# Optimization experiments

Measured on AMD Instinct MI355X. Metric: run time of the kernel, lower is better.

Reference implementation:

```python
import jax, jax.numpy as jnp
import numpy as np
import math

B, T, IN, H, OUT, L = 8, 256, 128, 128, 128, 2
MAX_EP_LEN = 10000.0


def _rotate(x, pos, d):
    # rope as in source: repeat(1,1,2) = concat along last dim (not interleave)
    half = jnp.exp(jnp.arange(0, d, 2, dtype=jnp.float32) * (-math.log(MAX_EP_LEN) / d))  # [d/2]
    ang = pos[..., None] * half  # [B,T,d/2]
    sine = jnp.concatenate([jnp.sin(ang), jnp.sin(ang)], axis=-1)
    cos = jnp.concatenate([jnp.cos(ang), jnp.cos(ang)], axis=-1)
    y1, y2 = jnp.split(x, 2, axis=-1)
    x_rot = jnp.concatenate([-y2, y1], axis=-1)
    return x * cos + x_rot * sine


def _layernorm(x, w, b, eps=1e-5):
    m = jnp.mean(x, axis=-1, keepdims=True)
    v = jnp.mean((x - m) ** 2, axis=-1, keepdims=True)
    return (x - m) / jnp.sqrt(v + eps) * w + b


def _block(x, S0, Z0, Wk, Wq, Wv, lw, lb, w1, b1, w2, b2, scw, scb):
    # x: [B,T,F]; S0: [B,F,F]; Z0: [B,F]
    x = _layernorm(x, lw, lb)
    K = jax.nn.elu(x @ Wk.T) + 1.0
    Q = jax.nn.elu(x @ Wq.T) + 1.0
    V = x @ Wv.T
    outer = jnp.einsum('bti,btj->btij', K, V)  # [B,T,F,F]
    S = jnp.clip(jnp.cumsum(outer, axis=1), -1e20, 1e20) + S0[:, None]  # [B,T,F,F]
    Z = jnp.clip(jnp.cumsum(K, axis=1), -1e20, 1e20) + Z0[:, None]      # [B,T,F]
    num = jnp.einsum('bti,btil->btl', Q, S)
    den = jnp.einsum('bti,bti->bt', Q, Z)[..., None] + 1e-5
    out = num / den
    out = jax.nn.relu(jax.nn.relu(out @ w1.T + b1) @ w2.T + b2)  # feed_forward
    out = out + x @ scw.T + scb                                   # residual shortcut
    return out, S[:, -1], Z[:, -1]


def setup_inputs() -> dict:
    key = jax.random.key(0)
    ks = jax.random.split(key, 14)
    s = 0.05
    return {
        'z': jax.random.normal(ks[0], (T, B, IN), jnp.float32),
        'state': jnp.zeros((B, L * (H * H + H) + 1), jnp.float32),
        'Wk': jax.random.normal(ks[1], (L, H, IN), jnp.float32) * s,
        'Wq': jax.random.normal(ks[2], (L, H, IN), jnp.float32) * s,
        'Wv': jax.random.normal(ks[3], (L, H, IN), jnp.float32) * s,
        'ln_w': jnp.ones((L, IN), jnp.float32),
        'ln_b': jnp.zeros((L, IN), jnp.float32),
        'ff_w1': jax.random.normal(ks[4], (L, H, H), jnp.float32) * s,
        'ff_b1': jnp.zeros((L, H), jnp.float32),
        'ff_w2': jax.random.normal(ks[5], (L, H, H), jnp.float32) * s,
        'ff_b2': jnp.zeros((L, H), jnp.float32),
        'sc_w': jax.random.normal(ks[6], (L, H, IN), jnp.float32) * s,
        'sc_b': jnp.zeros((L, H), jnp.float32),
        'unmap_w': jax.random.normal(ks[7], (OUT, H), jnp.float32) * s,
        'unmap_b': jnp.zeros((OUT,), jnp.float32),
    }


def reference(z, state, Wk, Wq, Wv, ln_w, ln_b, ff_w1, ff_b1, ff_w2, ff_b2, sc_w, sc_b, unmap_w, unmap_b):
    x = jnp.transpose(z, (1, 0, 2))  # [B,T,IN]
    ts = state[:, -1]                # [B] timestep counters
    core = state[:, :-1].reshape(B, L, H * H + H)
    pos = ts[:, None] + jnp.arange(T, dtype=jnp.float32)[None, :]  # [B,T]
    x = _rotate(x, pos, IN)  # embedding_type == 'rope'
    new_states = []
    for i in range(L):
        S0 = core[:, i, :H * H].reshape(B, H, H)
        Z0 = core[:, i, H * H:]
        x, Sl, Zl = _block(x, S0, Z0, Wk[i], Wq[i], Wv[i], ln_w[i], ln_b[i],
                           ff_w1[i], ff_b1[i], ff_w2[i], ff_b2[i], sc_w[i], sc_b[i])
        new_states.append(jnp.concatenate([Sl.reshape(B, -1), Zl], axis=-1))
    y = x @ unmap_w.T + unmap_b
    st = jnp.concatenate([jnp.stack(new_states, axis=1).reshape(B, -1), (ts + T)[:, None]], axis=-1)
    return jnp.transpose(y, (1, 0, 2)), st
```

## Files before the change

kernel.cpp:

```cpp
#include <hip/hip_runtime.h>
#include <math.h>

#define Bn 8
#define Tn 256
#define COREn 16512
#define SDn   33025

typedef __attribute__((ext_vector_type(8))) short short8;
typedef __attribute__((ext_vector_type(4))) short short4v;
typedef __attribute__((ext_vector_type(4))) float floatx4;

#define MFMA16(a,b,c) __builtin_amdgcn_mfma_f32_16x16x32_bf16(a,b,c,0,0,0)

static __device__ __forceinline__ unsigned short f2bf(float f) {
  unsigned int u = __float_as_uint(f);
  return (unsigned short)((u + 0x7FFFu + ((u >> 16) & 1u)) >> 16);
}
static __device__ __forceinline__ float bf2f(unsigned short h) {
  return __uint_as_float((unsigned int)h << 16);
}
static __device__ __forceinline__ short8 ldwfrag(const float* p) {
  float4 a = *(const float4*)p;
  float4 b = *(const float4*)(p + 4);
  short8 r;
  r[0] = (short)f2bf(a.x); r[1] = (short)f2bf(a.y);
  r[2] = (short)f2bf(a.z); r[3] = (short)f2bf(a.w);
  r[4] = (short)f2bf(b.x); r[5] = (short)f2bf(b.y);
  r[6] = (short)f2bf(b.z); r[7] = (short)f2bf(b.w);
  return r;
}
static __device__ __forceinline__ void ld8(const float* p, float* v) {
  float4 a = *(const float4*)p, b = *(const float4*)(p + 4);
  v[0]=a.x; v[1]=a.y; v[2]=a.z; v[3]=a.w; v[4]=b.x; v[5]=b.y; v[6]=b.z; v[7]=b.w;
}

struct Phase1 {
  unsigned short Ssc[4][16][40];
  float Obuf[4][16][132];
  float denw[4][16];
};
struct Phase2 {
  float sk[16][132];
  float os[16][132];
};
struct Smem {
  unsigned short xs[16][136];
  unsigned short xattn[16][136];
  unsigned short hs[16][136];
  float Z0s[128];
  float denz[16];
  float dinv[16];
  union { Phase1 p1; Phase2 p2; } u;
};

static __device__ __forceinline__ void proj_epilogue(
    int by, int g0, int b, int t0l, int n0, int n1, int quad,
    floatx4 acc0, floatx4 acc1,
    unsigned short* __restrict__ Kb, unsigned short* __restrict__ Kt,
    unsigned short* __restrict__ Qb, unsigned short* __restrict__ Vt,
    float* __restrict__ skipb, const float* __restrict__ scb) {
  if (by == 0) {
    short4v kt0, kt1;
#pragma unroll
    for (int j = 0; j < 4; j++) {
      int row = quad * 4 + j;
      float e0 = acc0[j] > 0.f ? acc0[j] + 1.f : expf(acc0[j]);
      float e1 = acc1[j] > 0.f ? acc1[j] + 1.f : expf(acc1[j]);
      Kb[(size_t)(g0 + row) * 128 + n0] = f2bf(e0);
      Kb[(size_t)(g0 + row) * 128 + n1] = f2bf(e1);
      kt0[j] = (short)f2bf(e0); kt1[j] = (short)f2bf(e1);
    }
    *(short4v*)(Kt + (size_t)(b * 128 + n0) * 256 + t0l + quad * 4) = kt0;
    *(short4v*)(Kt + (size_t)(b * 128 + n1) * 256 + t0l + quad * 4) = kt1;
  } else if (by == 1) {
#pragma unroll
    for (int j = 0; j < 4; j++) {
      int row = quad * 4 + j;
      float e0 = acc0[j] > 0.f ? acc0[j] + 1.f : expf(acc0[j]);
      float e1 = acc1[j] > 0.f ? acc1[j] + 1.f : expf(acc1[j]);
      Qb[(size_t)(g0 + row) * 128 + n0] = f2bf(e0);
      Qb[(size_t)(g0 + row) * 128 + n1] = f2bf(e1);
    }
  } else if (by == 2) {
    short4v v0, v1;
#pragma unroll
    for (int j = 0; j < 4; j++) { v0[j] = (short)f2bf(acc0[j]); v1[j] = (short)f2bf(acc1[j]); }
    *(short4v*)(Vt + (size_t)(b * 128 + n0) * 256 + t0l + quad * 4) = v0;
    *(short4v*)(Vt + (size_t)(b * 128 + n1) * 256 + t0l + quad * 4) = v1;
  } else {
    float sb0 = scb[n0], sb1 = scb[n1];
#pragma unroll
    for (int j = 0; j < 4; j++) {
      int row = quad * 4 + j;
      skipb[(size_t)(g0 + row) * 128 + n0] = acc0[j] + sb0;
      skipb[(size_t)(g0 + row) * 128 + n1] = acc1[j] + sb1;
    }
  }
}

static __device__ void attn_ff(
    Smem& s, int tid, int b, int rt, int l,
    const unsigned short* __restrict__ Kb, const unsigned short* __restrict__ Qb,
    const unsigned short* __restrict__ Vt,
    const float* __restrict__ state, const float* __restrict__ skipin,
    const float* __restrict__ w1, const float* __restrict__ b1,
    const float* __restrict__ w2, const float* __restrict__ b2,
    const float* __restrict__ Wk1, const float* __restrict__ Wq1,
    const float* __restrict__ Wv1, const float* __restrict__ scw1,
    const float* __restrict__ lnw1, const float* __restrict__ lnb1,
    const float* __restrict__ scb1,
    unsigned short* __restrict__ Kb1, unsigned short* __restrict__ Kt1,
    unsigned short* __restrict__ Qb1, unsigned short* __restrict__ Vt1,
    float* __restrict__ skip1,
    const float* __restrict__ unw, const float* __restrict__ unb,
    float* __restrict__ yout) {
  const int lane = tid & 63, wv = tid >> 6, lm = lane & 15, quad = lane >> 4;
  const int t0 = rt * 16;
  const size_t sb = (size_t)b * SDn + (size_t)l * COREn;

  { int r = tid >> 4, c = (tid & 15) * 8;
    *(short8*)&s.xs[r][c] = *(const short8*)(Qb + (size_t)(b * 256 + t0 + r) * 128 + c); }
  if (tid < 128) s.Z0s[tid] = state[sb + 16384 + tid];
  __syncthreads();

  { int r = tid >> 4, c = (tid & 15) * 8;
    float qz = 0.f;
#pragma unroll
    for (int i = 0; i < 8; i++) qz += bf2f(s.xs[r][c + i]) * s.Z0s[c + i];
    for (int d = 8; d; d >>= 1) qz += __shfl_xor(qz, d, 16);
    if ((tid & 15) == 0) s.denz[r] = qz; }

  floatx4 oacc[8];
#pragma unroll
  for (int jt = 0; jt < 8; jt++) oacc[jt] = floatx4{0.f, 0.f, 0.f, 0.f};
  float dacc[4] = {0.f, 0.f, 0.f, 0.f};

  const int nch = rt / 2 + 1;
  for (int c = wv; c < nch; c += 4) {
    const int kb = c * 32;
    floatx4 s0 = {0.f,0.f,0.f,0.f}, s1 = {0.f,0.f,0.f,0.f};
#pragma unroll
    for (int kc = 0; kc < 4; kc++) {
      short8 a  = *(const short8*)&s.xs[lm][kc * 32 + quad * 8];
      short8 k0 = *(const short8*)(Kb + (size_t)(b * 256 + kb + lm) * 128 + kc * 32 + quad * 8);
      short8 k1 = *(const short8*)(Kb + (size_t)(b * 256 + kb + 16 + lm) * 128 + kc * 32 + quad * 8);
      s0 = MFMA16(a, k0, s0);
      s1 = MFMA16(a, k1, s1);
    }
    const int tau0 = kb + lm, tau1 = kb + 16 + lm;
#pragma unroll
    for (int j = 0; j < 4; j++) {
      int m = t0 + quad * 4 + j;
      float v0 = (tau0 <= m) ? s0[j] : 0.f;
      float v1 = (tau1 <= m) ? s1[j] : 0.f;
      dacc[j] += v0 + v1;
      s.u.p1.Ssc[wv][quad * 4 + j][lm]      = f2bf(v0);
      s.u.p1.Ssc[wv][quad * 4 + j][16 + lm] = f2bf(v1);
    }
    short8 sa = *(const short8*)&s.u.p1.Ssc[wv][lm][quad * 8];
#pragma unroll
    for (int jt = 0; jt < 8; jt++) {
      short8 vb = *(const short8*)(Vt + (size_t)(b * 128 + jt * 16 + lm) * 256 + kb + quad * 8);
      oacc[jt] = MFMA16(sa, vb, oacc[jt]);
    }
  }

  { const float* S0 = state + sb;
    short8 aq = *(const short8*)&s.xs[lm][wv * 32 + quad * 8];
#pragma unroll
    for (int jt = 0; jt < 8; jt++) {
      short8 vb;
#pragma unroll
      for (int jj = 0; jj < 8; jj++)
        vb[jj] = (short)f2bf(S0[(size_t)(wv * 32 + quad * 8 + jj) * 128 + jt * 16 + lm]);
      oacc[jt] = MFMA16(aq, vb, oacc[jt]);
    } }

#pragma unroll
  for (int j = 0; j < 4; j++)
    for (int d = 8; d; d >>= 1) dacc[j] += __shfl_xor(dacc[j], d, 16);
  if (lm == 0) {
#pragma unroll
    for (int j = 0; j < 4; j++) s.u.p1.denw[wv][quad * 4 + j] = dacc[j];
  }
#pragma unroll
  for (int jt = 0; jt < 8; jt++)
#pragma unroll
    for (int j = 0; j < 4; j++)
      s.u.p1.Obuf[wv][quad * 4 + j][jt * 16 + lm] = oacc[jt][j];
  __syncthreads();
  if (tid < 16)
    s.dinv[tid] = 1.f / (s.denz[tid] + s.u.p1.denw[0][tid] + s.u.p1.denw[1][tid]
                         + s.u.p1.denw[2][tid] + s.u.p1.denw[3][tid] + 1e-5f);
  __syncthreads();
  { int r = tid >> 4, c = (tid & 15) * 8;
    float di = s.dinv[r];
    short8 ov;
#pragma unroll
    for (int i = 0; i < 8; i++) {
      float o = s.u.p1.Obuf[0][r][c + i] + s.u.p1.Obuf[1][r][c + i]
              + s.u.p1.Obuf[2][r][c + i] + s.u.p1.Obuf[3][r][c + i];
      ov[i] = (short)f2bf(o * di);
    }
    *(short8*)&s.xattn[r][c] = ov; }
  __syncthreads();

  const int gr0 = b * 256 + t0;
#pragma unroll
  for (int p = 0; p < 2; p++) {
    int f = tid + p * 256;
    int rr = f >> 5, cc = (f & 31) * 4;
    *(float4*)&s.u.p2.sk[rr][cc] = *(const float4*)(skipin + (size_t)(gr0 + rr) * 128 + cc);
  }
  const int n0 = wv * 32 + lm, n1 = n0 + 16;

  { floatx4 a0 = {0.f,0.f,0.f,0.f}, a1 = {0.f,0.f,0.f,0.f};
#pragma unroll
    for (int kc = 0; kc < 4; kc++) {
      short8 a  = *(const short8*)&s.xattn[lm][kc * 32 + quad * 8];
      short8 bA = ldwfrag(w1 + (size_t)n0 * 128 + kc * 32 + quad * 8);
      short8 bB = ldwfrag(w1 + (size_t)n1 * 128 + kc * 32 + quad * 8);
      a0 = MFMA16(a, bA, a0);
      a1 = MFMA16(a, bB, a1);
    }
    float bi0 = b1[n0], bi1 = b1[n1];
#pragma unroll
    for (int j = 0; j < 4; j++) {
      int row = quad * 4 + j;
      s.hs[row][n0] = f2bf(fmaxf(a0[j] + bi0, 0.f));
      s.hs[row][n1] = f2bf(fmaxf(a1[j] + bi1, 0.f));
    } }
  __syncthreads();

  float o0[4], o1[4];
  { floatx4 a0 = {0.f,0.f,0.f,0.f}, a1 = {0.f,0.f,0.f,0.f};
#pragma unroll
    for (int kc = 0; kc < 4; kc++) {
      short8 a  = *(const short8*)&s.hs[lm][kc * 32 + quad * 8];
      short8 bA = ldwfrag(w2 + (size_t)n0 * 128 + kc * 32 + quad * 8);
      short8 bB = ldwfrag(w2 + (size_t)n1 * 128 + kc * 32 + quad * 8);
      a0 = MFMA16(a, bA, a0);
      a1 = MFMA16(a, bB, a1);
    }
    float bi0 = b2[n0], bi1 = b2[n1];
#pragma unroll
    for (int j = 0; j < 4; j++) {
      int row = quad * 4 + j;
      o0[j] = fmaxf(a0[j] + bi0, 0.f) + s.u.p2.sk[row][n0];
      o1[j] = fmaxf(a1[j] + bi1, 0.f) + s.u.p2.sk[row][n1];
    } }

  if (l == 0) {
#pragma unroll
    for (int j = 0; j < 4; j++) {
      int row = quad * 4 + j;
      s.u.p2.os[row][n0] = o0[j];
      s.u.p2.os[row][n1] = o1[j];
    }
    __syncthreads();
    { int r = tid >> 4, c0 = (tid & 15) * 8;
      float v[8];
#pragma unroll
      for (int i = 0; i < 8; i++) v[i] = s.u.p2.os[r][c0 + i];
      float sm = 0.f, sq = 0.f;
#pragma unroll
      for (int i = 0; i < 8; i++) { sm += v[i]; sq += v[i] * v[i]; }
      for (int d = 8; d; d >>= 1) { sm += __shfl_xor(sm, d, 16); sq += __shfl_xor(sq, d, 16); }
      float mean = sm * (1.f / 128.f);
      float rstd = rsqrtf(sq * (1.f / 128.f) - mean * mean + 1e-5f);
      short8 xv;
#pragma unroll
      for (int i = 0; i < 8; i++)
        xv[i] = (short)f2bf((v[i] - mean) * rstd * lnw1[c0 + i] + lnb1[c0 + i]);
      *(short8*)&s.xs[r][c0] = xv; }
    __syncthreads();
#pragma unroll
    for (int by = 0; by < 4; by++) {
      const float* W = by == 0 ? Wk1 : by == 1 ? Wq1 : by == 2 ? Wv1 : scw1;
      floatx4 a0 = {0.f,0.f,0.f,0.f}, a1 = {0.f,0.f,0.f,0.f};
#pragma unroll
      for (int kc = 0; kc < 4; kc++) {
        short8 a  = *(const short8*)&s.xs[lm][kc * 32 + quad * 8];
        short8 bA = ldwfrag(W + (size_t)n0 * 128 + kc * 32 + quad * 8);
        short8 bB = ldwfrag(W + (size_t)n1 * 128 + kc * 32 + quad * 8);
        a0 = MFMA16(a, bA, a0);
        a1 = MFMA16(a, bB, a1);
      }
      proj_epilogue(by, gr0, b, t0, n0, n1, quad, a0, a1,
                    Kb1, Kt1, Qb1, Vt1, skip1, scb1);
    }
  } else {
#pragma unroll
    for (int j = 0; j < 4; j++) {
      int row = quad * 4 + j;
      s.xs[row][n0] = f2bf(o0[j]);
      s.xs[row][n1] = f2bf(o1[j]);
    }
    __syncthreads();
    floatx4 a0 = {0.f,0.f,0.f,0.f}, a1 = {0.f,0.f,0.f,0.f};
#pragma unroll
    for (int kc = 0; kc < 4; kc++) {
      short8 a  = *(const short8*)&s.xs[lm][kc * 32 + quad * 8];
      short8 bA = ldwfrag(unw + (size_t)n0 * 128 + kc * 32 + quad * 8);
      short8 bB = ldwfrag(unw + (size_t)n1 * 128 + kc * 32 + quad * 8);
      a0 = MFMA16(a, bA, a0);
      a1 = MFMA16(a, bB, a1);
    }
    float u0 = unb[n0], u1 = unb[n1];
#pragma unroll
    for (int j = 0; j < 4; j++) {
      int gg = gr0 + quad * 4 + j;
      int bb = gg >> 8, tq = gg & 255;
      yout[(size_t)(tq * Bn + bb) * 128 + n0] = a0[j] + u0;
      yout[(size_t)(tq * Bn + bb) * 128 + n1] = a1[j] + u1;
    }
  }
}

static __device__ void state_upd(
    int tid, int idx, int l,
    const unsigned short* __restrict__ Kt, const unsigned short* __restrict__ Vt,
    const float* __restrict__ state, float* __restrict__ st_out) {
  const int lane = tid & 63, wv = tid >> 6, lm = lane & 15, quad = lane >> 4;
  const int b = idx >> 4, sub = idx & 15;
  const int i0 = (sub >> 1) * 16, j0 = (sub & 1) * 64;
  const size_t sb = (size_t)b * SDn + (size_t)l * COREn;
  floatx4 acc = {0.f, 0.f, 0.f, 0.f};
#pragma unroll
  for (int kc = 0; kc < 8; kc++) {
    short8 ka = *(const short8*)(Kt + (size_t)(b * 128 + i0 + lm) * 256 + kc * 32 + quad * 8);
    short8 vb = *(const short8*)(Vt + (size_t)(b * 128 + j0 + wv * 16 + lm) * 256 + kc * 32 + quad * 8);
    acc = MFMA16(ka, vb, acc);
  }
#pragma unroll
  for (int j = 0; j < 4; j++) {
    size_t off = sb + (size_t)(i0 + quad * 4 + j) * 128 + j0 + wv * 16 + lm;
    st_out[off] = acc[j] + state[off];
  }
  if (j0 == 0) {
    if (tid < 128) {
      int i = tid >> 3, seg = tid & 7;
      const unsigned short* kr = Kt + (size_t)(b * 128 + i0 + i) * 256 + seg * 32;
      float zs = 0.f;
#pragma unroll
      for (int x = 0; x < 4; x++) {
        short8 kv = *(const short8*)(kr + x * 8);
#pragma unroll
        for (int y = 0; y < 8; y++) zs += bf2f((unsigned short)kv[y]);
      }
      for (int d = 4; d; d >>= 1) zs += __shfl_xor(zs, d, 8);
      if (seg == 0) {
        size_t zo = sb + 16384 + i0 + i;
        st_out[zo] = zs + state[zo];
      }
    }
    if (sub == 0 && tid == 0 && l == 0)
      st_out[(size_t)b * SDn + SDn - 1] = state[(size_t)b * SDn + SDn - 1] + 256.f;
  }
}

__global__ __launch_bounds__(256) void proj0_kernel(
    const float* __restrict__ z, const float* __restrict__ state,
    const float* __restrict__ Wk, const float* __restrict__ Wq,
    const float* __restrict__ Wv, const float* __restrict__ scw,
    const float* __restrict__ lnw, const float* __restrict__ lnb,
    const float* __restrict__ scb,
    unsigned short* __restrict__ Kb0, unsigned short* __restrict__ Qb0,
    unsigned short* __restrict__ Kt0, unsigned short* __restrict__ Vt0,
    float* __restrict__ skip0) {
  __shared__ unsigned short xs[16][136];
  const int tid = threadIdx.x, bx = blockIdx.x;
  const int lane = tid & 63, wv = tid >> 6, lm = lane & 15, quad = lane >> 4;
  const int tile = bx >> 1, half = bx & 1;
  const int g0 = tile * 16;
  const int r = tid >> 4, c0 = (tid & 15) * 8;
  const int g = g0 + r, b = g >> 8, t = g & 255;
  float v[8], pv[8];
  const float* zr = z + ((size_t)t * Bn + b) * 128;
  ld8(zr + c0, v);
  ld8(zr + (c0 ^ 64), pv);
  float pos = state[(size_t)b * SDn + SDn - 1] + (float)t;
#pragma unroll
  for (int i = 0; i < 8; i++) {
    int jj = (c0 + i) & 63;
    float ang = pos * expf((float)jj * -0.14391156831212787f);
    float sn = sinf(ang), cs = cosf(ang);
    v[i] = (c0 < 64) ? (v[i] * cs - pv[i] * sn) : (v[i] * cs + pv[i] * sn);
  }
  float sm = 0.f, sq = 0.f;
#pragma unroll
  for (int i = 0; i < 8; i++) { sm += v[i]; sq += v[i] * v[i]; }
  for (int d = 8; d; d >>= 1) { sm += __shfl_xor(sm, d, 16); sq += __shfl_xor(sq, d, 16); }
  float mean = sm * (1.f / 128.f);
  float rstd = rsqrtf(sq * (1.f / 128.f) - mean * mean + 1e-5f);
  short8 xv;
#pragma unroll
  for (int i = 0; i < 8; i++)
    xv[i] = (short)f2bf((v[i] - mean) * rstd * lnw[c0 + i] + lnb[c0 + i]);
  *(short8*)&xs[r][c0] = xv;
  __syncthreads();

  const int bb = g0 >> 8, t0l = g0 & 255;
  const int n0 = wv * 32 + lm, n1 = n0 + 16;
#pragma unroll
  for (int which = 0; which < 2; which++) {
    const float* W = half == 0 ? (which == 0 ? Wk : Wq)
                               : (which == 0 ? Wv : scw);
    floatx4 a0 = {0.f,0.f,0.f,0.f}, a1 = {0.f,0.f,0.f,0.f};
#pragma unroll
    for (int kc = 0; kc < 4; kc++) {
      short8 a  = *(const short8*)&xs[lm][kc * 32 + quad * 8];
      short8 bA = ldwfrag(W + (size_t)n0 * 128 + kc * 32 + quad * 8);
      short8 bB = ldwfrag(W + (size_t)n1 * 128 + kc * 32 + quad * 8);
      a0 = MFMA16(a, bA, a0);
      a1 = MFMA16(a, bB, a1);
    }
    proj_epilogue(half * 2 + which, g0, bb, t0l, n0, n1, quad, a0, a1,
                  Kb0, Kt0, Qb0, Vt0, skip0, scb);
  }
}

__global__ __launch_bounds__(256) void layer0_kernel(
    const unsigned short* __restrict__ Kb0, const unsigned short* __restrict__ Qb0,
    const unsigned short* __restrict__ Kt0, const unsigned short* __restrict__ Vt0,
    const float* __restrict__ skip0, const float* __restrict__ state,
    const float* __restrict__ w1, const float* __restrict__ b1,
    const float* __restrict__ w2, const float* __restrict__ b2,
    const float* __restrict__ Wk1, const float* __restrict__ Wq1,
    const float* __restrict__ Wv1, const float* __restrict__ scw1,
    const float* __restrict__ lnw1, const float* __restrict__ lnb1,
    const float* __restrict__ scb1,
    unsigned short* __restrict__ Kb1, unsigned short* __restrict__ Kt1,
    unsigned short* __restrict__ Qb1, unsigned short* __restrict__ Vt1,
    float* __restrict__ skip1, float* __restrict__ st_out) {
  __shared__ Smem s;
  const int tid = threadIdx.x, bx = blockIdx.x;
  if (bx < 128)
    attn_ff(s, tid, bx >> 4, bx & 15, 0,
            Kb0, Qb0, Vt0, state, skip0,
            w1, b1, w2, b2,
            Wk1, Wq1, Wv1, scw1, lnw1, lnb1, scb1,
            Kb1, Kt1, Qb1, Vt1, skip1,
            nullptr, nullptr, nullptr);
  else
    state_upd(tid, bx - 128, 0, Kt0, Vt0, state, st_out);
}

__global__ __launch_bounds__(256) void layer1_kernel(
    const unsigned short* __restrict__ Kb1, const unsigned short* __restrict__ Qb1,
    const unsigned short* __restrict__ Kt1, const unsigned short* __restrict__ Vt1,
    const float* __restrict__ skip1, const float* __restrict__ state,
    const float* __restrict__ w1, const float* __restrict__ b1,
    const float* __restrict__ w2, const float* __restrict__ b2,
    const float* __restrict__ unw, const float* __restrict__ unb,
    float* __restrict__ yout, float* __restrict__ st_out) {
  __shared__ Smem s;
  const int tid = threadIdx.x, bx = blockIdx.x;
  if (bx < 128)
    attn_ff(s, tid, bx >> 4, bx & 15, 1,
            Kb1, Qb1, Vt1, state, skip1,
            w1, b1, w2, b2,
            nullptr, nullptr, nullptr, nullptr, nullptr, nullptr, nullptr,
            nullptr, nullptr, nullptr, nullptr, nullptr,
            unw, unb, yout);
  else
    state_upd(tid, bx - 128, 1, Kt1, Vt1, state, st_out);
}

extern "C" void kernel_launch(void* const* d_in, const int* in_sizes, int n_in,
                              void* d_out, int out_size, void* d_ws, size_t ws_size,
                              hipStream_t stream) {
  const float* z       = (const float*)d_in[0];
  const float* state   = (const float*)d_in[1];
  const float* Wk      = (const float*)d_in[2];
  const float* Wq      = (const float*)d_in[3];
  const float* Wv      = (const float*)d_in[4];
  const float* ln_w    = (const float*)d_in[5];
  const float* ln_b    = (const float*)d_in[6];
  const float* ff_w1   = (const float*)d_in[7];
  const float* ff_b1   = (const float*)d_in[8];
  const float* ff_w2   = (const float*)d_in[9];
  const float* ff_b2   = (const float*)d_in[10];
  const float* sc_w    = (const float*)d_in[11];
  const float* sc_b    = (const float*)d_in[12];
  const float* unmap_w = (const float*)d_in[13];
  const float* unmap_b = (const float*)d_in[14];

  float* y_out  = (float*)d_out;
  float* st_out = y_out + (size_t)Tn * Bn * 128;

  const size_t E = 262144;
  unsigned short* Kb0 = (unsigned short*)d_ws;
  unsigned short* Qb0 = Kb0 + E;
  unsigned short* Kt0 = Qb0 + E;
  unsigned short* Vt0 = Kt0 + E;
  unsigned short* Kb1 = Vt0 + E;
  unsigned short* Qb1 = Kb1 + E;
  unsigned short* Kt1 = Qb1 + E;
  unsigned short* Vt1 = Kt1 + E;
  float* skip0 = (float*)(Vt1 + E);
  float* skip1 = skip0 + E;

  proj0_kernel<<<256, 256, 0, stream>>>(
      z, state, Wk, Wq, Wv, sc_w, ln_w, ln_b, sc_b,
      Kb0, Qb0, Kt0, Vt0, skip0);

  layer0_kernel<<<256, 256, 0, stream>>>(
      Kb0, Qb0, Kt0, Vt0, skip0, state,
      ff_w1, ff_b1, ff_w2, ff_b2,
      Wk + 16384, Wq + 16384, Wv + 16384, sc_w + 16384,
      ln_w + 128, ln_b + 128, sc_b + 128,
      Kb1, Kt1, Qb1, Vt1, skip1, st_out);

  layer1_kernel<<<256, 256, 0, stream>>>(
      Kb1, Qb1, Kt1, Vt1, skip1, state,
      ff_w1 + 16384, ff_b1 + 128, ff_w2 + 16384, ff_b2 + 128,
      unmap_w, unmap_b, y_out, st_out);
}
```

Baseline: 135.6 us.

## Split layer kernels into finer stages with more blocks and bf16 intermediates

Restructures the pipeline from three fat kernels into six stages: prep (rope+LN+projection plus a transposed bf16 copy of S0), attention split across two output-column halves, a separate feed-forward+LN kernel, a separate layer-1 projection kernel, and a fused FF+unmap kernel. The aim is more blocks per launch for better GPU occupancy, coalesced pre-transposed S0 reads instead of strided fp32 gathers, and bf16 skip storage to cut memory traffic. In exchange it adds more kernel launches, duplicates the QK score computation across the two halves, and round-trips attention output through global memory.

Result: faster. 130.4 us (-3.8%).

```diff
diff --git a/kernel.cpp b/kernel.cpp
--- a/kernel.cpp
+++ b/kernel.cpp
@@ -34,31 +34,12 @@
   v[0]=a.x; v[1]=a.y; v[2]=a.z; v[3]=a.w; v[4]=b.x; v[5]=b.y; v[6]=b.z; v[7]=b.w;
 }
 
-struct Phase1 {
-  unsigned short Ssc[4][16][40];
-  float Obuf[4][16][132];
-  float denw[4][16];
-};
-struct Phase2 {
-  float sk[16][132];
-  float os[16][132];
-};
-struct Smem {
-  unsigned short xs[16][136];
-  unsigned short xattn[16][136];
-  unsigned short hs[16][136];
-  float Z0s[128];
-  float denz[16];
-  float dinv[16];
-  union { Phase1 p1; Phase2 p2; } u;
-};
-
 static __device__ __forceinline__ void proj_epilogue(
     int by, int g0, int b, int t0l, int n0, int n1, int quad,
     floatx4 acc0, floatx4 acc1,
     unsigned short* __restrict__ Kb, unsigned short* __restrict__ Kt,
     unsigned short* __restrict__ Qb, unsigned short* __restrict__ Vt,
-    float* __restrict__ skipb, const float* __restrict__ scb) {
+    unsigned short* __restrict__ skipb, const float* __restrict__ scb) {
   if (by == 0) {
     short4v kt0, kt1;
 #pragma unroll
@@ -92,228 +73,88 @@
 #pragma unroll
     for (int j = 0; j < 4; j++) {
       int row = quad * 4 + j;
-      skipb[(size_t)(g0 + row) * 128 + n0] = acc0[j] + sb0;
-      skipb[(size_t)(g0 + row) * 128 + n1] = acc1[j] + sb1;
-    }
-  }
-}
-
-static __device__ void attn_ff(
-    Smem& s, int tid, int b, int rt, int l,
-    const unsigned short* __restrict__ Kb, const unsigned short* __restrict__ Qb,
-    const unsigned short* __restrict__ Vt,
-    const float* __restrict__ state, const float* __restrict__ skipin,
-    const float* __restrict__ w1, const float* __restrict__ b1,
-    const float* __restrict__ w2, const float* __restrict__ b2,
-    const float* __restrict__ Wk1, const float* __restrict__ Wq1,
-    const float* __restrict__ Wv1, const float* __restrict__ scw1,
-    const float* __restrict__ lnw1, const float* __restrict__ lnb1,
-    const float* __restrict__ scb1,
-    unsigned short* __restrict__ Kb1, unsigned short* __restrict__ Kt1,
-    unsigned short* __restrict__ Qb1, unsigned short* __restrict__ Vt1,
-    float* __restrict__ skip1,
-    const float* __restrict__ unw, const float* __restrict__ unb,
-    float* __restrict__ yout) {
-  const int lane = tid & 63, wv = tid >> 6, lm = lane & 15, quad = lane >> 4;
-  const int t0 = rt * 16;
-  const size_t sb = (size_t)b * SDn + (size_t)l * COREn;
-
-  { int r = tid >> 4, c = (tid & 15) * 8;
-    *(short8*)&s.xs[r][c] = *(const short8*)(Qb + (size_t)(b * 256 + t0 + r) * 128 + c); }
-  if (tid < 128) s.Z0s[tid] = state[sb + 16384 + tid];
-  __syncthreads();
-
-  { int r = tid >> 4, c = (tid & 15) * 8;
-    float qz = 0.f;
-#pragma unroll
-    for (int i = 0; i < 8; i++) qz += bf2f(s.xs[r][c + i]) * s.Z0s[c + i];
-    for (int d = 8; d; d >>= 1) qz += __shfl_xor(qz, d, 16);
-    if ((tid & 15) == 0) s.denz[r] = qz; }
-
-  floatx4 oacc[8];
-#pragma unroll
-  for (int jt = 0; jt < 8; jt++) oacc[jt] = floatx4{0.f, 0.f, 0.f, 0.f};
-  float dacc[4] = {0.f, 0.f, 0.f, 0.f};
-
-  const int nch = rt / 2 + 1;
-  for (int c = wv; c < nch; c += 4) {
-    const int kb = c * 32;
-    floatx4 s0 = {0.f,0.f,0.f,0.f}, s1 = {0.f,0.f,0.f,0.f};
+      skipb[(size_t)(g0 + row) * 128 + n0] = f2bf(acc0[j] + sb0);
+      skipb[(size_t)(g0 + row) * 128 + n1] = f2bf(acc1[j] + sb1);
+    }
+  }
+}
+
+__global__ __launch_bounds__(256) void prep_kernel(
+    const float* __restrict__ z, const float* __restrict__ state,
+    const float* __restrict__ Wk, const float* __restrict__ Wq,
+    const float* __restrict__ Wv, const float* __restrict__ scw,
+    const float* __restrict__ lnw, const float* __restrict__ lnb,
+    const float* __restrict__ scb,
+    unsigned short* __restrict__ Kb0, unsigned short* __restrict__ Qb0,
+    unsigned short* __restrict__ Kt0, unsigned short* __restrict__ Vt0,
+    unsigned short* __restrict__ skip0, unsigned short* __restrict__ S0t) {
+  const int tid = threadIdx.x, bx = blockIdx.x;
+  if (bx < 512) {
+    __shared__ unsigned short xs[16][136];
+    const int lane = tid & 63, wv = tid >> 6, lm = lane & 15, quad = lane >> 4;
+    const int tile = bx >> 2, by = bx & 3;
+    const int g0 = tile * 16;
+    const int r = tid >> 4, c0 = (tid & 15) * 8;
+    const int g = g0 + r, b = g >> 8, t = g & 255;
+    float v[8], pv[8];
+    const float* zr = z + ((size_t)t * Bn + b) * 128;
+    ld8(zr + c0, v);
+    ld8(zr + (c0 ^ 64), pv);
+    float pos = state[(size_t)b * SDn + SDn - 1] + (float)t;
+#pragma unroll
+    for (int i = 0; i < 8; i++) {
+      int jj = (c0 + i) & 63;
+      float ang = pos * expf((float)jj * -0.14391156831212787f);
+      float sn = sinf(ang), cs = cosf(ang);
+      v[i] = (c0 < 64) ? (v[i] * cs - pv[i] * sn) : (v[i] * cs + pv[i] * sn);
+    }
+    float sm = 0.f, sq = 0.f;
+#pragma unroll
+    for (int i = 0; i < 8; i++) { sm += v[i]; sq += v[i] * v[i]; }
+    for (int d = 8; d; d >>= 1) { sm += __shfl_xor(sm, d, 16); sq += __shfl_xor(sq, d, 16); }
+    float mean = sm * (1.f / 128.f);
+    float rstd = rsqrtf(sq * (1.f / 128.f) - mean * mean + 1e-5f);
+    short8 xv;
+#pragma unroll
+    for (int i = 0; i < 8; i++)
+      xv[i] = (short)f2bf((v[i] - mean) * rstd * lnw[c0 + i] + lnb[c0 + i]);
+    *(short8*)&xs[r][c0] = xv;
+    __syncthreads();
+
+    const float* W = by == 0 ? Wk : by == 1 ? Wq : by == 2 ? Wv : scw;
+    const int bb = g0 >> 8, t0l = g0 & 255;
+    const int n0 = wv * 32 + lm, n1 = n0 + 16;
+    floatx4 a0 = {0.f,0.f,0.f,0.f}, a1 = {0.f,0.f,0.f,0.f};
 #pragma unroll
     for (int kc = 0; kc < 4; kc++) {
-      short8 a  = *(const short8*)&s.xs[lm][kc * 32 + quad * 8];
-      short8 k0 = *(const short8*)(Kb + (size_t)(b * 256 + kb + lm) * 128 + kc * 32 + quad * 8);
-      short8 k1 = *(const short8*)(Kb + (size_t)(b * 256 + kb + 16 + lm) * 128 + kc * 32 + quad * 8);
-      s0 = MFMA16(a, k0, s0);
-      s1 = MFMA16(a, k1, s1);
-    }
-    const int tau0 = kb + lm, tau1 = kb + 16 + lm;
-#pragma unroll
-    for (int j = 0; j < 4; j++) {
-      int m = t0 + quad * 4 + j;
-      float v0 = (tau0 <= m) ? s0[j] : 0.f;
-      float v1 = (tau1 <= m) ? s1[j] : 0.f;
-      dacc[j] += v0 + v1;
-      s.u.p1.Ssc[wv][quad * 4 + j][lm]      = f2bf(v0);
-      s.u.p1.Ssc[wv][quad * 4 + j][16 + lm] = f2bf(v1);
-    }
-    short8 sa = *(const short8*)&s.u.p1.Ssc[wv][lm][quad * 8];
-#pragma unroll
-    for (int jt = 0; jt < 8; jt++) {
-      short8 vb = *(const short8*)(Vt + (size_t)(b * 128 + jt * 16 + lm) * 256 + kb + quad * 8);
-      oacc[jt] = MFMA16(sa, vb, oacc[jt]);
-    }
-  }
-
-  { const float* S0 = state + sb;
-    short8 aq = *(const short8*)&s.xs[lm][wv * 32 + quad * 8];
-#pragma unroll
-    for (int jt = 0; jt < 8; jt++) {
-      short8 vb;
-#pragma unroll
-      for (int jj = 0; jj < 8; jj++)
-        vb[jj] = (short)f2bf(S0[(size_t)(wv * 32 + quad * 8 + jj) * 128 + jt * 16 + lm]);
-      oacc[jt] = MFMA16(aq, vb, oacc[jt]);
-    } }
-
-#pragma unroll
-  for (int j = 0; j < 4; j++)
-    for (int d = 8; d; d >>= 1) dacc[j] += __shfl_xor(dacc[j], d, 16);
-  if (lm == 0) {
-#pragma unroll
-    for (int j = 0; j < 4; j++) s.u.p1.denw[wv][quad * 4 + j] = dacc[j];
-  }
-#pragma unroll
-  for (int jt = 0; jt < 8; jt++)
-#pragma unroll
-    for (int j = 0; j < 4; j++)
-      s.u.p1.Obuf[wv][quad * 4 + j][jt * 16 + lm] = oacc[jt][j];
-  __syncthreads();
-  if (tid < 16)
-    s.dinv[tid] = 1.f / (s.denz[tid] + s.u.p1.denw[0][tid] + s.u.p1.denw[1][tid]
-                         + s.u.p1.denw[2][tid] + s.u.p1.denw[3][tid] + 1e-5f);
-  __syncthreads();
-  { int r = tid >> 4, c = (tid & 15) * 8;
-    float di = s.dinv[r];
-    short8 ov;
-#pragma unroll
-    for (int i = 0; i < 8; i++) {
-      float o = s.u.p1.Obuf[0][r][c + i] + s.u.p1.Obuf[1][r][c + i]
-              + s.u.p1.Obuf[2][r][c + i] + s.u.p1.Obuf[3][r][c + i];
-      ov[i] = (short)f2bf(o * di);
-    }
-    *(short8*)&s.xattn[r][c] = ov; }
-  __syncthreads();
-
-  const int gr0 = b * 256 + t0;
-#pragma unroll
-  for (int p = 0; p < 2; p++) {
-    int f = tid + p * 256;
-    int rr = f >> 5, cc = (f & 31) * 4;
-    *(float4*)&s.u.p2.sk[rr][cc] = *(const float4*)(skipin + (size_t)(gr0 + rr) * 128 + cc);
-  }
-  const int n0 = wv * 32 + lm, n1 = n0 + 16;
-
-  { floatx4 a0 = {0.f,0.f,0.f,0.f}, a1 = {0.f,0.f,0.f,0.f};
-#pragma unroll
-    for (int kc = 0; kc < 4; kc++) {
-      short8 a  = *(const short8*)&s.xattn[lm][kc * 32 + quad * 8];
-      short8 bA = ldwfrag(w1 + (size_t)n0 * 128 + kc * 32 + quad * 8);
-      short8 bB = ldwfrag(w1 + (size_t)n1 * 128 + kc * 32 + quad * 8);
+      short8 a  = *(const short8*)&xs[lm][kc * 32 + quad * 8];
+      short8 bA = ldwfrag(W + (size_t)n0 * 128 + kc * 32 + quad * 8);
+      short8 bB = ldwfrag(W + (size_t)n1 * 128 + kc * 32 + quad * 8);
       a0 = MFMA16(a, bA, a0);
       a1 = MFMA16(a, bB, a1);
     }
-    float bi0 = b1[n0], bi1 = b1[n1];
-#pragma unroll
-    for (int j = 0; j < 4; j++) {
-      int row = quad * 4 + j;
-      s.hs[row][n0] = f2bf(fmaxf(a0[j] + bi0, 0.f));
-      s.hs[row][n1] = f2bf(fmaxf(a1[j] + bi1, 0.f));
-    } }
-  __syncthreads();
-
-  float o0[4], o1[4];
-  { floatx4 a0 = {0.f,0.f,0.f,0.f}, a1 = {0.f,0.f,0.f,0.f};
-#pragma unroll
-    for (int kc = 0; kc < 4; kc++) {
-      short8 a  = *(const short8*)&s.hs[lm][kc * 32 + quad * 8];
-      short8 bA = ldwfrag(w2 + (size_t)n0 * 128 + kc * 32 + quad * 8);
-      short8 bB = ldwfrag(w2 + (size_t)n1 * 128 + kc * 32 + quad * 8);
-      a0 = MFMA16(a, bA, a0);
-      a1 = MFMA16(a, bB, a1);
-    }
-    float bi0 = b2[n0], bi1 = b2[n1];
-#pragma unroll
-    for (int j = 0; j < 4; j++) {
-      int row = quad * 4 + j;
-      o0[j] = fmaxf(a0[j] + bi0, 0.f) + s.u.p2.sk[row][n0];
-      o1[j] = fmaxf(a1[j] + bi1, 0.f) + s.u.p2.sk[row][n1];
-    } }
-
-  if (l == 0) {
-#pragma unroll
-    for (int j = 0; j < 4; j++) {
-      int row = quad * 4 + j;
-      s.u.p2.os[row][n0] = o0[j];
-      s.u.p2.os[row][n1] = o1[j];
-    }
-    __syncthreads();
-    { int r = tid >> 4, c0 = (tid & 15) * 8;
-      float v[8];
-#pragma unroll
-      for (int i = 0; i < 8; i++) v[i] = s.u.p2.os[r][c0 + i];
-      float sm = 0.f, sq = 0.f;
-#pragma unroll
-      for (int i = 0; i < 8; i++) { sm += v[i]; sq += v[i] * v[i]; }
-      for (int d = 8; d; d >>= 1) { sm += __shfl_xor(sm, d, 16); sq += __shfl_xor(sq, d, 16); }
-      float mean = sm * (1.f / 128.f);
-      float rstd = rsqrtf(sq * (1.f / 128.f) - mean * mean + 1e-5f);
-      short8 xv;
-#pragma unroll
-      for (int i = 0; i < 8; i++)
-        xv[i] = (short)f2bf((v[i] - mean) * rstd * lnw1[c0 + i] + lnb1[c0 + i]);
-      *(short8*)&s.xs[r][c0] = xv; }
-    __syncthreads();
-#pragma unroll
-    for (int by = 0; by < 4; by++) {
-      const float* W = by == 0 ? Wk1 : by == 1 ? Wq1 : by == 2 ? Wv1 : scw1;
-      floatx4 a0 = {0.f,0.f,0.f,0.f}, a1 = {0.f,0.f,0.f,0.f};
-#pragma unroll
-      for (int kc = 0; kc < 4; kc++) {
-        short8 a  = *(const short8*)&s.xs[lm][kc * 32 + quad * 8];
-        short8 bA = ldwfrag(W + (size_t)n0 * 128 + kc * 32 + quad * 8);
-        short8 bB = ldwfrag(W + (size_t)n1 * 128 + kc * 32 + quad * 8);
-        a0 = MFMA16(a, bA, a0);
-        a1 = MFMA16(a, bB, a1);
+    proj_epilogue(by, g0, bb, t0l, n0, n1, quad, a0, a1,
+                  Kb0, Kt0, Qb0, Vt0, skip0, scb);
+  } else {
+    __shared__ float tl[32][33];
+    const int id = bx - 512, b = id >> 1, l = id & 1;
+    const float* src = state + (size_t)b * SDn + (size_t)l * COREn;
+    unsigned short* dst = S0t + (size_t)(l * 8 + b) * 16384;
+    const int r = tid >> 3, c4 = (tid & 7) * 4;
+#pragma unroll
+    for (int tI = 0; tI < 4; tI++)
+      for (int tJ = 0; tJ < 4; tJ++) {
+        int i0 = tI * 32, j0 = tJ * 32;
+#pragma unroll
+        for (int q = 0; q < 4; q++)
+          tl[r][c4 + q] = src[(size_t)(i0 + r) * 128 + j0 + c4 + q];
+        __syncthreads();
+        short4v o;
+#pragma unroll
+        for (int q = 0; q < 4; q++) o[q] = (short)f2bf(tl[c4 + q][r]);
+        *(short4v*)(dst + (size_t)(j0 + r) * 128 + i0 + c4) = o;
+        __syncthreads();
       }
-      proj_epilogue(by, gr0, b, t0, n0, n1, quad, a0, a1,
-                    Kb1, Kt1, Qb1, Vt1, skip1, scb1);
-    }
-  } else {
-#pragma unroll
-    for (int j = 0; j < 4; j++) {
-      int row = quad * 4 + j;
-      s.xs[row][n0] = f2bf(o0[j]);
-      s.xs[row][n1] = f2bf(o1[j]);
-    }
-    __syncthreads();
-    floatx4 a0 = {0.f,0.f,0.f,0.f}, a1 = {0.f,0.f,0.f,0.f};
-#pragma unroll
-    for (int kc = 0; kc < 4; kc++) {
-      short8 a  = *(const short8*)&s.xs[lm][kc * 32 + quad * 8];
-      short8 bA = ldwfrag(unw + (size_t)n0 * 128 + kc * 32 + quad * 8);
-      short8 bB = ldwfrag(unw + (size_t)n1 * 128 + kc * 32 + quad * 8);
-      a0 = MFMA16(a, bA, a0);
-      a1 = MFMA16(a, bB, a1);
-    }
-    float u0 = unb[n0], u1 = unb[n1];
-#pragma unroll
-    for (int j = 0; j < 4; j++) {
-      int gg = gr0 + quad * 4 + j;
-      int bb = gg >> 8, tq = gg & 255;
-      yout[(size_t)(tq * Bn + bb) * 128 + n0] = a0[j] + u0;
-      yout[(size_t)(tq * Bn + bb) * 128 + n1] = a1[j] + u1;
-    }
   }
 }
 
@@ -359,112 +200,310 @@
   }
 }
 
-__global__ __launch_bounds__(256) void proj0_kernel(
-    const float* __restrict__ z, const float* __restrict__ state,
+__global__ __launch_bounds__(256) void attn_kernel(
+    const unsigned short* __restrict__ Kb, const unsigned short* __restrict__ Qb,
+    const unsigned short* __restrict__ Vt, const unsigned short* __restrict__ Kt,
+    const unsigned short* __restrict__ S0tl, const float* __restrict__ state,
+    unsigned short* __restrict__ attnb, float* __restrict__ st_out, int l) {
+  const int tid = threadIdx.x, bx = blockIdx.x;
+  const int lane = tid & 63, wv = tid >> 6, lm = lane & 15, quad = lane >> 4;
+  if (bx < 256) {
+    __shared__ unsigned short xs[16][136];
+    __shared__ unsigned short Ssc[4][16][40];
+    __shared__ float Obuf[4][16][68];
+    __shared__ float Z0s[128];
+    __shared__ float denw[4][16];
+    __shared__ float denz[16];
+    __shared__ float dinv[16];
+
+    const int tile = bx >> 1, half = bx & 1;
+    const int b = tile >> 4, rt = tile & 15, t0 = rt * 16;
+    const size_t sb = (size_t)b * SDn + (size_t)l * COREn;
+    { int r = tid >> 4, c = (tid & 15) * 8;
+      *(short8*)&xs[r][c] = *(const short8*)(Qb + (size_t)(b * 256 + t0 + r) * 128 + c); }
+    if (tid < 128) Z0s[tid] = state[sb + 16384 + tid];
+    __syncthreads();
+
+    { int r = tid >> 4, c = (tid & 15) * 8;
+      float qz = 0.f;
+#pragma unroll
+      for (int i = 0; i < 8; i++) qz += bf2f(xs[r][c + i]) * Z0s[c + i];
+      for (int d = 8; d; d >>= 1) qz += __shfl_xor(qz, d, 16);
+      if ((tid & 15) == 0) denz[r] = qz; }
+
+    floatx4 oacc[4];
+#pragma unroll
+    for (int jt = 0; jt < 4; jt++) oacc[jt] = floatx4{0.f, 0.f, 0.f, 0.f};
+    float dacc[4] = {0.f, 0.f, 0.f, 0.f};
+
+    const int nch = rt / 2 + 1;
+    for (int c = wv; c < nch; c += 4) {
+      const int kb = c * 32;
+      short8 vfr[4];
+#pragma unroll
+      for (int jt = 0; jt < 4; jt++)
+        vfr[jt] = *(const short8*)(Vt + (size_t)(b * 128 + half * 64 + jt * 16 + lm) * 256 + kb + quad * 8);
+      floatx4 s0 = {0.f,0.f,0.f,0.f}, s1 = {0.f,0.f,0.f,0.f};
+#pragma unroll
+      for (int kc = 0; kc < 4; kc++) {
+        short8 a  = *(const short8*)&xs[lm][kc * 32 + quad * 8];
+        short8 k0 = *(const short8*)(Kb + (size_t)(b * 256 + kb + lm) * 128 + kc * 32 + quad * 8);
+        short8 k1 = *(const short8*)(Kb + (size_t)(b * 256 + kb + 16 + lm) * 128 + kc * 32 + quad * 8);
+        s0 = MFMA16(a, k0, s0);
+        s1 = MFMA16(a, k1, s1);
+      }
+      const int tau0 = kb + lm, tau1 = kb + 16 + lm;
+#pragma unroll
+      for (int j = 0; j < 4; j++) {
+        int m = t0 + quad * 4 + j;
+        float v0 = (tau0 <= m) ? s0[j] : 0.f;
+        float v1 = (tau1 <= m) ? s1[j] : 0.f;
+        dacc[j] += v0 + v1;
+        Ssc[wv][quad * 4 + j][lm]      = f2bf(v0);
+        Ssc[wv][quad * 4 + j][16 + lm] = f2bf(v1);
+      }
+      short8 sa = *(const short8*)&Ssc[wv][lm][quad * 8];
+#pragma unroll
+      for (int jt = 0; jt < 4; jt++)
+        oacc[jt] = MFMA16(sa, vfr[jt], oacc[jt]);
+    }
+
+    { short8 aq = *(const short8*)&xs[lm][wv * 32 + quad * 8];
+#pragma unroll
+      for (int jt = 0; jt < 4; jt++) {
+        short8 vb = *(const short8*)(S0tl + (size_t)b * 16384 +
+                        (size_t)(half * 64 + jt * 16 + lm) * 128 + wv * 32 + quad * 8);
+        oacc[jt] = MFMA16(aq, vb, oacc[jt]);
+      } }
+
+#pragma unroll
+    for (int j = 0; j < 4; j++)
+      for (int d = 8; d; d >>= 1) dacc[j] += __shfl_xor(dacc[j], d, 16);
+    if (lm == 0) {
+#pragma unroll
+      for (int j = 0; j < 4; j++) denw[wv][quad * 4 + j] = dacc[j];
+    }
+#pragma unroll
+    for (int jt = 0; jt < 4; jt++)
+#pragma unroll
+      for (int j = 0; j < 4; j++)
+        Obuf[wv][quad * 4 + j][jt * 16 + lm] = oacc[jt][j];
+    __syncthreads();
+    if (tid < 16)
+      dinv[tid] = 1.f / (denz[tid] + denw[0][tid] + denw[1][tid]
+                         + denw[2][tid] + denw[3][tid] + 1e-5f);
+    __syncthreads();
+    { int r = tid >> 4, c = (tid & 15) * 4;
+      float di = dinv[r];
+      short4v ov;
+#pragma unroll
+      for (int q = 0; q < 4; q++) {
+        float o = Obuf[0][r][c + q] + Obuf[1][r][c + q]
+                + Obuf[2][r][c + q] + Obuf[3][r][c + q];
+        ov[q] = (short)f2bf(o * di);
+      }
+      *(short4v*)(attnb + (size_t)(b * 256 + t0 + r) * 128 + half * 64 + c) = ov; }
+  } else {
+    state_upd(tid, bx - 256, l, Kt, Vt, state, st_out);
+  }
+}
+
+__global__ __launch_bounds__(256) void ffln_kernel(
+    const unsigned short* __restrict__ attnb, const unsigned short* __restrict__ skipb,
+    const float* __restrict__ w1, const float* __restrict__ b1,
+    const float* __restrict__ w2, const float* __restrict__ b2,
+    const float* __restrict__ lnw1, const float* __restrict__ lnb1,
+    unsigned short* __restrict__ xln1) {
+  __shared__ unsigned short xa[16][136];
+  __shared__ unsigned short hs[16][136];
+  __shared__ float os[16][132];
+  const int tid = threadIdx.x, g0 = blockIdx.x * 16;
+  const int lane = tid & 63, wv = tid >> 6, lm = lane & 15, quad = lane >> 4;
+  const int n0 = wv * 32 + lm, n1 = n0 + 16;
+
+  short8 w1A[4], w1B[4], w2A[4], w2B[4];
+#pragma unroll
+  for (int kc = 0; kc < 4; kc++) {
+    w1A[kc] = ldwfrag(w1 + (size_t)n0 * 128 + kc * 32 + quad * 8);
+    w1B[kc] = ldwfrag(w1 + (size_t)n1 * 128 + kc * 32 + quad * 8);
+    w2A[kc] = ldwfrag(w2 + (size_t)n0 * 128 + kc * 32 + quad * 8);
+    w2B[kc] = ldwfrag(w2 + (size_t)n1 * 128 + kc * 32 + quad * 8);
+  }
+  float bi10 = b1[n0], bi11 = b1[n1], bi20 = b2[n0], bi21 = b2[n1];
+  float sk0[4], sk1[4];
+#pragma unroll
+  for (int j = 0; j < 4; j++) {
+    sk0[j] = bf2f(skipb[(size_t)(g0 + quad * 4 + j) * 128 + n0]);
+    sk1[j] = bf2f(skipb[(size_t)(g0 + quad * 4 + j) * 128 + n1]);
+  }
+  { int r = tid >> 4, c = (tid & 15) * 8;
+    *(short8*)&xa[r][c] = *(const short8*)(attnb + (size_t)(g0 + r) * 128 + c); }
+  __syncthreads();
+
+  { floatx4 a0 = {0.f,0.f,0.f,0.f}, a1 = {0.f,0.f,0.f,0.f};
+#pragma unroll
+    for (int kc = 0; kc < 4; kc++) {
+      short8 a = *(const short8*)&xa[lm][kc * 32 + quad * 8];
+      a0 = MFMA16(a, w1A[kc], a0);
+      a1 = MFMA16(a, w1B[kc], a1);
+    }
+#pragma unroll
+    for (int j = 0; j < 4; j++) {
+      int row = quad * 4 + j;
+      hs[row][n0] = f2bf(fmaxf(a0[j] + bi10, 0.f));
+      hs[row][n1] = f2bf(fmaxf(a1[j] + bi11, 0.f));
+    } }
+  __syncthreads();
+  { floatx4 a0 = {0.f,0.f,0.f,0.f}, a1 = {0.f,0.f,0.f,0.f};
+#pragma unroll
+    for (int kc = 0; kc < 4; kc++) {
+      short8 a = *(const short8*)&hs[lm][kc * 32 + quad * 8];
+      a0 = MFMA16(a, w2A[kc], a0);
+      a1 = MFMA16(a, w2B[kc], a1);
+    }
+#pragma unroll
+    for (int j = 0; j < 4; j++) {
+      int row = quad * 4 + j;
+      os[row][n0] = fmaxf(a0[j] + bi20, 0.f) + sk0[j];
+      os[row][n1] = fmaxf(a1[j] + bi21, 0.f) + sk1[j];
+    } }
+  __syncthreads();
+  { int r = tid >> 4, c0 = (tid & 15) * 8;
+    float v[8];
+#pragma unroll
+    for (int i = 0; i < 8; i++) v[i] = os[r][c0 + i];
+    float sm = 0.f, sq = 0.f;
+#pragma unroll
+    for (int i = 0; i < 8; i++) { sm += v[i]; sq += v[i] * v[i]; }
+    for (int d = 8; d; d >>= 1) { sm += __shfl_xor(sm, d, 16); sq += __shfl_xor(sq, d, 16); }
+    float mean = sm * (1.f / 128.f);
+    float rstd = rsqrtf(sq * (1.f / 128.f) - mean * mean + 1e-5f);
+    short8 xv;
+#pragma unroll
+    for (int i = 0; i < 8; i++)
+      xv[i] = (short)f2bf((v[i] - mean) * rstd * lnw1[c0 + i] + lnb1[c0 + i]);
+    *(short8*)(xln1 + (size_t)(g0 + r) * 128 + c0) = xv; }
+}
+
+__global__ __launch_bounds__(256) void proj1_kernel(
+    const unsigned short* __restrict__ xln1,
     const float* __restrict__ Wk, const float* __restrict__ Wq,
     const float* __restrict__ Wv, const float* __restrict__ scw,
-    const float* __restrict__ lnw, const float* __restrict__ lnb,
     const float* __restrict__ scb,
-    unsigned short* __restrict__ Kb0, unsigned short* __restrict__ Qb0,
-    unsigned short* __restrict__ Kt0, unsigned short* __restrict__ Vt0,
-    float* __restrict__ skip0) {
+    unsigned short* __restrict__ Kb1, unsigned short* __restrict__ Qb1,
+    unsigned short* __restrict__ Kt1, unsigned short* __restrict__ Vt1,
+    unsigned short* __restrict__ skip1) {
   __shared__ unsigned short xs[16][136];
   const int tid = threadIdx.x, bx = blockIdx.x;
   const int lane = tid & 63, wv = tid >> 6, lm = lane & 15, quad = lane >> 4;
-  const int tile = bx >> 1, half = bx & 1;
+  const int tile = bx >> 2, by = bx & 3;
   const int g0 = tile * 16;
-  const int r = tid >> 4, c0 = (tid & 15) * 8;
-  const int g = g0 + r, b = g >> 8, t = g & 255;
-  float v[8], pv[8];
-  const float* zr = z + ((size_t)t * Bn + b) * 128;
-  ld8(zr + c0, v);
-  ld8(zr + (c0 ^ 64), pv);
-  float pos = state[(size_t)b * SDn + SDn - 1] + (float)t;
-#pragma unroll
-  for (int i = 0; i < 8; i++) {
-    int jj = (c0 + i) & 63;
-    float ang = pos * expf((float)jj * -0.14391156831212787f);
-    float sn = sinf(ang), cs = cosf(ang);
-    v[i] = (c0 < 64) ? (v[i] * cs - pv[i] * sn) : (v[i] * cs + pv[i] * sn);
-  }
-  float sm = 0.f, sq = 0.f;
-#pragma unroll
-  for (int i = 0; i < 8; i++) { sm += v[i]; sq += v[i] * v[i]; }
-  for (int d = 8; d; d >>= 1) { sm += __shfl_xor(sm, d, 16); sq += __shfl_xor(sq, d, 16); }
-  float mean = sm * (1.f / 128.f);
-  float rstd = rsqrtf(sq * (1.f / 128.f) - mean * mean + 1e-5f);
-  short8 xv;
-#pragma unroll
-  for (int i = 0; i < 8; i++)
-    xv[i] = (short)f2bf((v[i] - mean) * rstd * lnw[c0 + i] + lnb[c0 + i]);
-  *(short8*)&xs[r][c0] = xv;
-  __syncthreads();
-
+  { int r = tid >> 4, c = (tid & 15) * 8;
+    *(short8*)&xs[r][c] = *(const short8*)(xln1 + (size_t)(g0 + r) * 128 + c); }
+  __syncthreads();
+  const float* W = by == 0 ? Wk : by == 1 ? Wq : by == 2 ? Wv : scw;
   const int bb = g0 >> 8, t0l = g0 & 255;
   const int n0 = wv * 32 + lm, n1 = n0 + 16;
-#pragma unroll
-  for (int which = 0; which < 2; which++) {
-    const float* W = half == 0 ? (which == 0 ? Wk : Wq)
-                               : (which == 0 ? Wv : scw);
-    floatx4 a0 = {0.f,0.f,0.f,0.f}, a1 = {0.f,0.f,0.f,0.f};
-#pragma unroll
-    for (int kc = 0; kc < 4; kc++) {
-      short8 a  = *(const short8*)&xs[lm][kc * 32 + quad * 8];
-      short8 bA = ldwfrag(W + (size_t)n0 * 128 + kc * 32 + quad * 8);
-      short8 bB = ldwfrag(W + (size_t)n1 * 128 + kc * 32 + quad * 8);
-      a0 = MFMA16(a, bA, a0);
-      a1 = MFMA16(a, bB, a1);
-    }
-    proj_epilogue(half * 2 + which, g0, bb, t0l, n0, n1, quad, a0, a1,
-                  Kb0, Kt0, Qb0, Vt0, skip0, scb);
-  }
-}
-
-__global__ __launch_bounds__(256) void layer0_kernel(
-    const unsigned short* __restrict__ Kb0, const unsigned short* __restrict__ Qb0,
-    const unsigned short* __restrict__ Kt0, const unsigned short* __restrict__ Vt0,
-    const float* __restrict__ skip0, const float* __restrict__ state,
-    const float* __restrict__ w1, const float* __restrict__ b1,
-    const float* __restrict__ w2, const float* __restrict__ b2,
-    const float* __restrict__ Wk1, const float* __restrict__ Wq1,
-    const float* __restrict__ Wv1, const float* __restrict__ scw1,
-    const float* __restrict__ lnw1, const float* __restrict__ lnb1,
-    const float* __restrict__ scb1,
-    unsigned short* __restrict__ Kb1, unsigned short* __restrict__ Kt1,
-    unsigned short* __restrict__ Qb1, unsigned short* __restrict__ Vt1,
-    float* __restrict__ skip1, float* __restrict__ st_out) {
-  __shared__ Smem s;
-  const int tid = threadIdx.x, bx = blockIdx.x;
-  if (bx < 128)
-    attn_ff(s, tid, bx >> 4, bx & 15, 0,
-            Kb0, Qb0, Vt0, state, skip0,
-            w1, b1, w2, b2,
-            Wk1, Wq1, Wv1, scw1, lnw1, lnb1, scb1,
-            Kb1, Kt1, Qb1, Vt1, skip1,
-            nullptr, nullptr, nullptr);
-  else
-    state_upd(tid, bx - 128, 0, Kt0, Vt0, state, st_out);
-}
-
-__global__ __launch_bounds__(256) void layer1_kernel(
-    const unsigned short* __restrict__ Kb1, const unsigned short* __restrict__ Qb1,
-    const unsigned short* __restrict__ Kt1, const unsigned short* __restrict__ Vt1,
-    const float* __restrict__ skip1, const float* __restrict__ state,
+  floatx4 a0 = {0.f,0.f,0.f,0.f}, a1 = {0.f,0.f,0.f,0.f};
+#pragma unroll
+  for (int kc = 0; kc < 4; kc++) {
+    short8 a  = *(const short8*)&xs[lm][kc * 32 + quad * 8];
+    short8 bA = ldwfrag(W + (size_t)n0 * 128 + kc * 32 + quad * 8);
+    short8 bB = ldwfrag(W + (size_t)n1 * 128 + kc * 32 + quad * 8);
+    a0 = MFMA16(a, bA, a0);
+    a1 = MFMA16(a, bB, a1);
+  }
+  proj_epilogue(by, g0, bb, t0l, n0, n1, quad, a0, a1,
+                Kb1, Kt1, Qb1, Vt1, skip1, scb);
+}
+
+__global__ __launch_bounds__(256) void ffu_kernel(
+    const unsigned short* __restrict__ attnb, const unsigned short* __restrict__ skipb,
     const float* __restrict__ w1, const float* __restrict__ b1,
     const float* __restrict__ w2, const float* __restrict__ b2,
     const float* __restrict__ unw, const float* __restrict__ unb,
-    float* __restrict__ yout, float* __restrict__ st_out) {
-  __shared__ Smem s;
-  const int tid = threadIdx.x, bx = blockIdx.x;
-  if (bx < 128)
-    attn_ff(s, tid, bx >> 4, bx & 15, 1,
-            Kb1, Qb1, Vt1, state, skip1,
-            w1, b1, w2, b2,
-            nullptr, nullptr, nullptr, nullptr, nullptr, nullptr, nullptr,
-            nullptr, nullptr, nullptr, nullptr, nullptr,
-            unw, unb, yout);
-  else
-    state_upd(tid, bx - 128, 1, Kt1, Vt1, state, st_out);
+    float* __restrict__ yout) {
+  __shared__ unsigned short xa[16][136];
+  __shared__ unsigned short hs[16][136];
+  const int tid = threadIdx.x, g0 = blockIdx.x * 16;
+  const int lane = tid & 63, wv = tid >> 6, lm = lane & 15, quad = lane >> 4;
+  const int n0 = wv * 32 + lm, n1 = n0 + 16;
+
+  short8 w1A[4], w1B[4], w2A[4], w2B[4];
+#pragma unroll
+  for (int kc = 0; kc < 4; kc++) {
+    w1A[kc] = ldwfrag(w1 + (size_t)n0 * 128 + kc * 32 + quad * 8);
+    w1B[kc] = ldwfrag(w1 + (size_t)n1 * 128 + kc * 32 + quad * 8);
+    w2A[kc] = ldwfrag(w2 + (size_t)n0 * 128 + kc * 32 + quad * 8);
+    w2B[kc] = ldwfrag(w2 + (size_t)n1 * 128 + kc * 32 + quad * 8);
+  }
+  float bi10 = b1[n0], bi11 = b1[n1], bi20 = b2[n0], bi21 = b2[n1];
+  float sk0[4], sk1[4];
+#pragma unroll
+  for (int j = 0; j < 4; j++) {
+    sk0[j] = bf2f(skipb[(size_t)(g0 + quad * 4 + j) * 128 + n0]);
+    sk1[j] = bf2f(skipb[(size_t)(g0 + quad * 4 + j) * 128 + n1]);
+  }
+  { int r = tid >> 4, c = (tid & 15) * 8;
+    *(short8*)&xa[r][c] = *(const short8*)(attnb + (size_t)(g0 + r) * 128 + c); }
+  __syncthreads();
+
+  { floatx4 a0 = {0.f,0.f,0.f,0.f}, a1 = {0.f,0.f,0.f,0.f};
+#pragma unroll
+    for (int kc = 0; kc < 4; kc++) {
+      short8 a = *(const short8*)&xa[lm][kc * 32 + quad * 8];
+      a0 = MFMA16(a, w1A[kc], a0);
+      a1 = MFMA16(a, w1B[kc], a1);
+    }
+#pragma unroll
+    for (int j = 0; j < 4; j++) {
+      int row = quad * 4 + j;
+      hs[row][n0] = f2bf(fmaxf(a0[j] + bi10, 0.f));
+      hs[row][n1] = f2bf(fmaxf(a1[j] + bi11, 0.f));
+    } }
+  __syncthreads();
+  short8 uA[4], uB[4];
+#pragma unroll
+  for (int kc = 0; kc < 4; kc++) {
+    uA[kc] = ldwfrag(unw + (size_t)n0 * 128 + kc * 32 + quad * 8);
+    uB[kc] = ldwfrag(unw + (size_t)n1 * 128 + kc * 32 + quad * 8);
+  }
+  float o0[4], o1[4];
+  { floatx4 a0 = {0.f,0.f,0.f,0.f}, a1 = {0.f,0.f,0.f,0.f};
+#pragma unroll
+    for (int kc = 0; kc < 4; kc++) {
+      short8 a = *(const short8*)&hs[lm][kc * 32 + quad * 8];
+      a0 = MFMA16(a, w2A[kc], a0);
+      a1 = MFMA16(a, w2B[kc], a1);
+    }
+#pragma unroll
+    for (int j = 0; j < 4; j++) {
+      o0[j] = fmaxf(a0[j] + bi20, 0.f) + sk0[j];
+      o1[j] = fmaxf(a1[j] + bi21, 0.f) + sk1[j];
+    } }
+  __syncthreads();
+#pragma unroll
+  for (int j = 0; j < 4; j++) {
+    int row = quad * 4 + j;
+    hs[row][n0] = f2bf(o0[j]);
+    hs[row][n1] = f2bf(o1[j]);
+  }
+  __syncthreads();
+  { floatx4 a0 = {0.f,0.f,0.f,0.f}, a1 = {0.f,0.f,0.f,0.f};
+#pragma unroll
+    for (int kc = 0; kc < 4; kc++) {
+      short8 a = *(const short8*)&hs[lm][kc * 32 + quad * 8];
+      a0 = MFMA16(a, uA[kc], a0);
+      a1 = MFMA16(a, uB[kc], a1);
+    }
+    float u0 = unb[n0], u1 = unb[n1];
+#pragma unroll
+    for (int j = 0; j < 4; j++) {
+      int gg = g0 + quad * 4 + j;
+      int bb = gg >> 8, tq = gg & 255;
+      yout[(size_t)(tq * Bn + bb) * 128 + n0] = a0[j] + u0;
+      yout[(size_t)(tq * Bn + bb) * 128 + n1] = a1[j] + u1;
+    } }
 }
 
 extern "C" void kernel_launch(void* const* d_in, const int* in_sizes, int n_in,
@@ -490,30 +529,39 @@
   float* st_out = y_out + (size_t)Tn * Bn * 128;
 
   const size_t E = 262144;
-  unsigned short* Kb0 = (unsigned short*)d_ws;
-  unsigned short* Qb0 = Kb0 + E;
-  unsigned short* Kt0 = Qb0 + E;
-  unsigned short* Vt0 = Kt0 + E;
-  unsigned short* Kb1 = Vt0 + E;
-  unsigned short* Qb1 = Kb1 + E;
-  unsigned short* Kt1 = Qb1 + E;
-  unsigned short* Vt1 = Kt1 + E;
-  float* skip0 = (float*)(Vt1 + E);
-  float* skip1 = skip0 + E;
-
-  proj0_kernel<<<256, 256, 0, stream>>>(
+  unsigned short* Kb0  = (unsigned short*)d_ws;
+  unsigned short* Qb0  = Kb0 + E;
+  unsigned short* Kt0  = Qb0 + E;
+  unsigned short* Vt0  = Kt0 + E;
+  unsigned short* Kb1  = Vt0 + E;
+  unsigned short* Qb1  = Kb1 + E;
+  unsigned short* Kt1  = Qb1 + E;
+  unsigned short* Vt1  = Kt1 + E;
+  unsigned short* skip0 = Vt1 + E;
+  unsigned short* skip1 = skip0 + E;
+  unsigned short* attnb = skip1 + E;
+  unsigned short* xln1  = attnb + E;
+  unsigned short* S0t   = xln1 + E;
+
+  prep_kernel<<<528, 256, 0, stream>>>(
       z, state, Wk, Wq, Wv, sc_w, ln_w, ln_b, sc_b,
-      Kb0, Qb0, Kt0, Vt0, skip0);
-
-  layer0_kernel<<<256, 256, 0, stream>>>(
-      Kb0, Qb0, Kt0, Vt0, skip0, state,
-      ff_w1, ff_b1, ff_w2, ff_b2,
-      Wk + 16384, Wq + 16384, Wv + 16384, sc_w + 16384,
-      ln_w + 128, ln_b + 128, sc_b + 128,
-      Kb1, Kt1, Qb1, Vt1, skip1, st_out);
-
-  layer1_kernel<<<256, 256, 0, stream>>>(
-      Kb1, Qb1, Kt1, Vt1, skip1, state,
-      ff_w1 + 16384, ff_b1 + 128, ff_w2 + 16384, ff_b2 + 128,
-      unmap_w, unmap_b, y_out, st_out);
-}
+      Kb0, Qb0, Kt0, Vt0, skip0, S0t);
+
+  attn_kernel<<<384, 256, 0, stream>>>(
+      Kb0, Qb0, Vt0, Kt0, S0t, state, attnb, st_out, 0);
+
+  ffln_kernel<<<128, 256, 0, stream>>>(
+      attnb, skip0, ff_w1, ff_b1, ff_w2, ff_b2,
+      ln_w + 128, ln_b + 128, xln1);
+
+  proj1_kernel<<<512, 256, 0, stream>>>(
+      xln1, Wk + 16384, Wq + 16384, Wv + 16384, sc_w + 16384, sc_b + 128,
+      Kb1, Qb1, Kt1, Vt1, skip1);
+
+  attn_kernel<<<384, 256, 0, stream>>>(
+      Kb1, Qb1, Vt1, Kt1, S0t + (size_t)8 * 16384, state, attnb, st_out, 1);
+
+  ffu_kernel<<<128, 256, 0, stream>>>(
+      attnb, skip1, ff_w1 + 16384, ff_b1 + 128, ff_w2 + 16384, ff_b2 + 128,
+      unmap_w, unmap_b, y_out);
+}
```
